# Optimization experiments

Measured on AMD Instinct MI355X. Metric: run time of the kernel, lower is better.

The kernel has to match this reference:

```python
import jax, jax.numpy as jnp
import numpy as np

N = 100000  # nodes
E = 320000  # edges
G = 64      # graphs in the batch


def setup_inputs() -> dict:
    key = jax.random.key(0)
    ks = jax.random.split(key, 16)
    inp = {
        "x": jax.random.normal(ks[0], (N, 512), dtype=jnp.float32),
        "edge_index": jax.random.randint(ks[1], (2, E), 0, N, dtype=jnp.int64),
        "batch": jnp.sort(jax.random.randint(ks[2], (N,), 0, G, dtype=jnp.int64)),
    }
    # GCNConv weights (in, out) and biases, Glorot-ish scale
    dims = [(512, 256), (256, 128), (128, 64), (64, 32)]
    for i, (din, dout) in enumerate(dims):
        inp[f"w{i+1}"] = jax.random.normal(ks[3 + i], (din, dout), dtype=jnp.float32) / np.sqrt(din)
        inp[f"b{i+1}"] = jnp.zeros((dout,), dtype=jnp.float32)
    inp["lw1"] = jax.random.normal(ks[8], (32, 16), dtype=jnp.float32) / np.sqrt(32.0)
    inp["lb1"] = jnp.zeros((16,), dtype=jnp.float32)
    inp["lw2"] = jax.random.normal(ks[9], (16, 2), dtype=jnp.float32) / np.sqrt(16.0)
    inp["lb2"] = jnpp = jnp.zeros((2,), dtype=jnp.float32)
    return inp


def _gcn_conv(h_in, w, b, src, dst, norm, n):
    # x' = D^-1/2 (A+I) D^-1/2 (X W) + b   (PyG GCNConv default)
    h = h_in @ w                                  # [N, out]
    msg = h[src] * norm[:, None]                  # gather + scale over edges(+self-loops)
    out = jax.ops.segment_sum(msg, dst, num_segments=n)  # scatter-add
    return out + b


def reference(x, edge_index, batch, w1, b1, w2, b2, w3, b3, w4, b4, lw1, lb1, lw2, lb2):
    n = x.shape[0]
    loop = jnp.arange(n, dtype=edge_index.dtype)
    src = jnp.concatenate([edge_index[0], loop])  # add self-loops
    dst = jnp.concatenate([edge_index[1], loop])
    # symmetric normalization: deg counted at dst (col) including self-loops
    deg = jax.ops.segment_sum(jnp.ones_like(dst, dtype=x.dtype), dst, num_segments=n)
    dinv = jnp.where(deg > 0, 1.0 / jnp.sqrt(deg), 0.0)
    norm = dinv[src] * dinv[dst]                  # [E+N]

    h = jax.nn.relu(_gcn_conv(x, w1, b1, src, dst, norm, n))
    h = jax.nn.relu(_gcn_conv(h, w2, b2, src, dst, norm, n))
    h = jax.nn.relu(_gcn_conv(h, w3, b3, src, dst, norm, n))
    h = _gcn_conv(h, w4, b4, src, dst, norm, n)   # [N, 32]

    # global mean pool over graphs
    sums = jax.ops.segment_sum(h, batch, num_segments=G)
    cnt = jax.ops.segment_sum(jnp.ones((n,), dtype=h.dtype), batch, num_segments=G)
    pooled = sums / jnp.maximum(cnt, 1.0)[:, None]  # [G, 32]

    # dropout p=0.8 is identity in eval mode
    out = jax.nn.relu(pooled @ lw1 + lb1) @ lw2 + lb2  # [G, 2]
    return out
```

## Files before the change

kernel.cpp:

```cpp
#include <hip/hip_runtime.h>
#include <cstdint>
#include <cstddef>


typedef __attribute__((ext_vector_type(8))) short s16x8;
typedef __attribute__((ext_vector_type(4))) float f32x4;

__device__ __forceinline__ short2 split2(float f) {
    union { float f; unsigned u; } c; c.f = f;
    short hi = (short)(c.u >> 16);
    union { unsigned u; float f; } h; h.u = c.u & 0xffff0000u;
    union { float f; unsigned u; } r; r.f = f - h.f;
    short lo = (short)(r.u >> 16);
    return make_short2(hi, lo);
}

__device__ __forceinline__ void gload16(const void* g, void* l) {
    __builtin_amdgcn_global_load_lds(
        (const __attribute__((address_space(1))) unsigned int*)g,
        (__attribute__((address_space(3))) unsigned int*)l, 16, 0, 0);
}


__global__ void k_count(const int* __restrict__ dst, int E, int* __restrict__ cnt) {
    int e = blockIdx.x * blockDim.x + threadIdx.x;
    if (e < E) atomicAdd(&cnt[dst[e]], 1);
}

__global__ void k_dinv(const int* __restrict__ cnt, int n, float* __restrict__ dinv) {
    int i = blockIdx.x * blockDim.x + threadIdx.x;
    if (i < n) dinv[i] = rsqrtf((float)(cnt[i] + 1));
}

__global__ void k_scan_sums(const int* __restrict__ cnt, int n, int* __restrict__ bsum) {
    __shared__ int s[256];
    int t = threadIdx.x;
    int base = blockIdx.x * 4096 + t * 16;
    int sum = 0;
#pragma unroll
    for (int j = 0; j < 16; ++j) { int i = base + j; if (i < n) sum += cnt[i]; }
    s[t] = sum;
    __syncthreads();
    for (int off = 128; off > 0; off >>= 1) {
        if (t < off) s[t] += s[t + off];
        __syncthreads();
    }
    if (t == 0) bsum[blockIdx.x] = s[0];
}

__global__ void k_scan_offsets(const int* __restrict__ bsum, int nb,
                               int* __restrict__ boff, int* __restrict__ totalp) {
    int t = threadIdx.x;
    int v = (t < nb) ? bsum[t] : 0;
    int x = v;
    for (int off = 1; off < 64; off <<= 1) {
        int y = __shfl_up(x, off);
        if (t >= off) x += y;
    }
    if (t < nb) boff[t] = x - v;
    if (t == 63) *totalp = x;
}

__global__ void k_scan_final(const int* __restrict__ cnt, int n,
                             const int* __restrict__ boff, int* __restrict__ row_ptr) {
    __shared__ int s[256];
    int t = threadIdx.x;
    int base = blockIdx.x * 4096 + t * 16;
    int v[16]; int sum = 0;
#pragma unroll
    for (int j = 0; j < 16; ++j) { int i = base + j; v[j] = (i < n) ? cnt[i] : 0; sum += v[j]; }
    s[t] = sum;
    __syncthreads();
    for (int off = 1; off < 256; off <<= 1) {
        int y = (t >= off) ? s[t - off] : 0;
        __syncthreads();
        s[t] += y;
        __syncthreads();
    }
    int run = boff[blockIdx.x] + ((t == 0) ? 0 : s[t - 1]);
#pragma unroll
    for (int j = 0; j < 16; ++j) {
        int i = base + j;
        if (i < n) row_ptr[i] = run;
        run += v[j];
    }
}

__global__ void k_fill(const int* __restrict__ src, const int* __restrict__ dst, int E,
                       const int* __restrict__ row_ptr, int* __restrict__ cursor,
                       int* __restrict__ csr_src) {
    int e = blockIdx.x * blockDim.x + threadIdx.x;
    if (e >= E) return;
    int d = dst[e];
    int p = atomicAdd(&cursor[d], 1);
    csr_src[row_ptr[d] + p] = src[e];
}


__global__ void k_split_w(const float* __restrict__ w, int N, int total, int kshift,
                          unsigned short* __restrict__ th, unsigned short* __restrict__ tl) {
    int idx = blockIdx.x * blockDim.x + threadIdx.x;
    if (idx >= total) return;
    int nn = idx >> kshift;
    int k  = idx & ((1 << kshift) - 1);
    short2 p = split2(w[(size_t)k * N + nn]);
    th[idx] = (unsigned short)p.x;
    tl[idx] = (unsigned short)p.y;
}


template <int FN, bool SPLIT_A>
__global__ __launch_bounds__(256)
void k_gemm(const float* __restrict__ A32,
            const unsigned short* __restrict__ Ah, const unsigned short* __restrict__ Al,
            const unsigned short* __restrict__ Bth, const unsigned short* __restrict__ Btl,
            float* __restrict__ C, int M, int K, int N) {
    constexpr int FM = 4;
    constexpr int BM = 128;
    constexpr int BN = FN * 32;
    constexpr int ABYTES = BM * 64;
    constexpr int BBYTES = BN * 64;
    constexpr int BUF = 2 * ABYTES + 2 * BBYTES;
    __shared__ char lds[2 * BUF];

    const int tid  = threadIdx.x;
    const int lane = tid & 63;
    const int w    = tid >> 6;
    const int wm   = w & 1;
    const int wn   = w >> 1;
    const int brow = blockIdx.y * BM;
    const int bcol = blockIdx.x * BN;
    const int l15  = lane & 15;
    const int kb   = (lane >> 4) * 16;

    const int arow_t = tid >> 1;
    const int ahalf  = tid & 1;
    int arow_g = brow + arow_t; if (arow_g > M - 1) arow_g = M - 1;
    const float* xrow = A32 + (size_t)arow_g * K + ahalf * 16;

    f32x4 acc[FM][FN];
#pragma unroll
    for (int i = 0; i < FM; ++i)
#pragma unroll
        for (int j = 0; j < FN; ++j) acc[i][j] = (f32x4){0.f, 0.f, 0.f, 0.f};

    const int KT = K / 32;
    float4 xr0, xr1, xr2, xr3;

    auto loadX = [&](int k0) {
        const float4* p = (const float4*)(xrow + k0);
        xr0 = p[0]; xr1 = p[1]; xr2 = p[2]; xr3 = p[3];
    };
    auto writeA = [&](char* base) {
        float v[16] = {xr0.x, xr0.y, xr0.z, xr0.w, xr1.x, xr1.y, xr1.z, xr1.w,
                       xr2.x, xr2.y, xr2.z, xr2.w, xr3.x, xr3.y, xr3.z, xr3.w};
        s16x8 h0, h1, l0, l1;
#pragma unroll
        for (int j = 0; j < 8; ++j) { short2 q = split2(v[j]);     h0[j] = q.x; l0[j] = q.y; }
#pragma unroll
        for (int j = 0; j < 8; ++j) { short2 q = split2(v[8 + j]); h1[j] = q.x; l1[j] = q.y; }
        int vq = (arow_t >> 1) & 3;
        int q0 = (2 * ahalf) ^ vq;
        int q1 = (2 * ahalf + 1) ^ vq;
        char* sAh = base;
        char* sAl = base + ABYTES;
        *(s16x8*)(sAh + arow_t * 64 + q0 * 16) = h0;
        *(s16x8*)(sAh + arow_t * 64 + q1 * 16) = h1;
        *(s16x8*)(sAl + arow_t * 64 + q0 * 16) = l0;
        *(s16x8*)(sAl + arow_t * 64 + q1 * 16) = l1;
    };
    auto stageAg = [&](char* base, int k0) {
#pragma unroll
        for (int u = 0; u < 4; ++u) {
            int id = w + u * 4;
            int hi = (id < 8) ? 1 : 0;
            int s  = hi ? id : id - 8;
            int p  = s * 64 + lane;
            int kq = (p ^ ((p >> 3) & 3)) & 3;
            int row = p >> 2;
            const unsigned short* gs = (hi ? Ah : Al) + (size_t)(brow + row) * K + k0 + kq * 8;
            gload16(gs, base + (hi ? 0 : ABYTES) + s * 1024);
        }
    };
    auto stageB = [&](char* base, int k0) {
        char* sBh = base + 2 * ABYTES;
        char* sBl = sBh + BBYTES;
#pragma unroll
        for (int u = 0; u < BN / 32; ++u) {
            int id = w + u * 4;
            int hi = (id < BN / 16) ? 1 : 0;
            int s  = hi ? id : id - BN / 16;
            int p  = s * 64 + lane;
            int kq = (p ^ ((p >> 3) & 3)) & 3;
            int col = p >> 2;
            const unsigned short* gs = (hi ? Bth : Btl) + (size_t)(bcol + col) * K + k0 + kq * 8;
            gload16(gs, (hi ? sBh : sBl) + s * 1024);
        }
    };

    char* cur = lds;
    char* nxt = lds + BUF;
    if constexpr (SPLIT_A) loadX(0);
    stageB(cur, 0);
    if constexpr (SPLIT_A) writeA(cur); else stageAg(cur, 0);
    __syncthreads();

    for (int t = 0; t < KT; ++t) {
        const int k1 = (t + 1) * 32;
        const bool more = (t + 1 < KT);
        if (more) {
            if constexpr (SPLIT_A) loadX(k1);
            stageB(nxt, k1);
            if constexpr (!SPLIT_A) stageAg(nxt, k1);
        }

        {
            char* sAh = cur;
            char* sAl = cur + ABYTES;
            char* sBh = cur + 2 * ABYTES;
            char* sBl = sBh + BBYTES;
            s16x8 fah[FM], fam[FM];
#pragma unroll
            for (int i = 0; i < FM; ++i) {
                int row = wm * 64 + i * 16 + l15;
                int o = row * 64 + (kb ^ (((row >> 1) & 3) << 4));
                fah[i] = *(const s16x8*)(sAh + o);
                fam[i] = *(const s16x8*)(sAl + o);
            }
#pragma unroll
            for (int j = 0; j < FN; ++j) {
                int col = wn * FN * 16 + j * 16 + l15;
                int o = col * 64 + (kb ^ (((col >> 1) & 3) << 4));
                s16x8 fbh = *(const s16x8*)(sBh + o);
                s16x8 fbm = *(const s16x8*)(sBl + o);
#pragma unroll
                for (int i = 0; i < FM; ++i) {
                    acc[i][j] = __builtin_amdgcn_mfma_f32_16x16x32_bf16(fah[i], fbh, acc[i][j], 0, 0, 0);
                    acc[i][j] = __builtin_amdgcn_mfma_f32_16x16x32_bf16(fam[i], fbh, acc[i][j], 0, 0, 0);
                    acc[i][j] = __builtin_amdgcn_mfma_f32_16x16x32_bf16(fah[i], fbm, acc[i][j], 0, 0, 0);
                }
            }
        }

        if constexpr (SPLIT_A) {
            if (more) writeA(nxt);
        }
        __syncthreads();
        char* tmp = cur; cur = nxt; nxt = tmp;
    }

#pragma unroll
    for (int i = 0; i < FM; ++i) {
#pragma unroll
        for (int r = 0; r < 4; ++r) {
            int row = brow + wm * 64 + i * 16 + (lane >> 4) * 4 + r;
            if (row >= M) continue;
#pragma unroll
            for (int j = 0; j < FN; ++j) {
                int col = bcol + wn * FN * 16 + j * 16 + l15;
                C[(size_t)row * N + col] = acc[i][j][r];
            }
        }
    }
}


__global__ void k_agg_split(const float4* __restrict__ h, const int* __restrict__ row_ptr,
                            const int* __restrict__ csr_src, const float* __restrict__ dinv,
                            const float* __restrict__ bias,
                            unsigned short* __restrict__ oh, unsigned short* __restrict__ ol,
                            int n, int f_shift) {
    int idx = blockIdx.x * blockDim.x + threadIdx.x;
    int dout4 = 1 << f_shift;
    int total = n << f_shift;
    if (idx >= total) return;
    int i = idx >> f_shift;
    int f = idx & (dout4 - 1);

    float di = dinv[i];
    float4 hv = h[(size_t)i * dout4 + f];
    float4 acc;
    acc.x = hv.x * di; acc.y = hv.y * di; acc.z = hv.z * di; acc.w = hv.w * di;

    int s0 = row_ptr[i], s1 = row_ptr[i + 1];
    for (int e = s0; e < s1; ++e) {
        int s = csr_src[e];
        float ds = dinv[s];
        float4 v = h[(size_t)s * dout4 + f];
        acc.x += v.x * ds; acc.y += v.y * ds; acc.z += v.z * ds; acc.w += v.w * ds;
    }
    const float4* b4 = (const float4*)bias;
    float4 b = b4[f];
    float4 o;
    o.x = fmaxf(acc.x * di + b.x, 0.f);
    o.y = fmaxf(acc.y * di + b.y, 0.f);
    o.z = fmaxf(acc.z * di + b.z, 0.f);
    o.w = fmaxf(acc.w * di + b.w, 0.f);

    short2 p0 = split2(o.x), p1 = split2(o.y), p2 = split2(o.z), p3 = split2(o.w);
    size_t base = ((size_t)i << f_shift << 2) + f * 4;
    *(ushort4*)(oh + base) = make_ushort4((unsigned short)p0.x, (unsigned short)p1.x,
                                          (unsigned short)p2.x, (unsigned short)p3.x);
    *(ushort4*)(ol + base) = make_ushort4((unsigned short)p0.y, (unsigned short)p1.y,
                                          (unsigned short)p2.y, (unsigned short)p3.y);
}


__global__ void k_agg(const float4* __restrict__ h, const int* __restrict__ row_ptr,
                      const int* __restrict__ csr_src, const float* __restrict__ dinv,
                      const float* __restrict__ bias, float4* __restrict__ out,
                      int n, int f_shift) {
    int idx = blockIdx.x * blockDim.x + threadIdx.x;
    int dout4 = 1 << f_shift;
    int total = n << f_shift;
    if (idx >= total) return;
    int i = idx >> f_shift;
    int f = idx & (dout4 - 1);

    float di = dinv[i];
    float4 hv = h[(size_t)i * dout4 + f];
    float4 acc;
    acc.x = hv.x * di; acc.y = hv.y * di; acc.z = hv.z * di; acc.w = hv.w * di;

    int s0 = row_ptr[i], s1 = row_ptr[i + 1];
    for (int e = s0; e < s1; ++e) {
        int s = csr_src[e];
        float ds = dinv[s];
        float4 v = h[(size_t)s * dout4 + f];
        acc.x += v.x * ds; acc.y += v.y * ds; acc.z += v.z * ds; acc.w += v.w * ds;
    }
    const float4* b4 = (const float4*)bias;
    float4 b = b4[f];
    float4 o;
    o.x = acc.x * di + b.x;
    o.y = acc.y * di + b.y;
    o.z = acc.z * di + b.z;
    o.w = acc.w * di + b.w;
    out[(size_t)i * dout4 + f] = o;
}


__global__ void k_pool(const float* __restrict__ h, const int* __restrict__ batch,
                       int n, float* __restrict__ pooled) {
    int g = blockIdx.x;
    int start, end;
    {
        int lo = 0, hi = n;
        while (lo < hi) { int mid = (lo + hi) >> 1; if (batch[mid] < g) lo = mid + 1; else hi = mid; }
        start = lo;
        lo = start; hi = n;
        while (lo < hi) { int mid = (lo + hi) >> 1; if (batch[mid] < g + 1) lo = mid + 1; else hi = mid; }
        end = lo;
    }
    int f = threadIdx.x & 31;
    int sub = threadIdx.x >> 5;
    float s = 0.f;
    for (int i = start + sub; i < end; i += 8) s += h[(size_t)i * 32 + f];
    __shared__ float red[8][32];
    red[sub][f] = s;
    __syncthreads();
    if (sub == 0) {
        float t = 0.f;
#pragma unroll
        for (int k = 0; k < 8; ++k) t += red[k][f];
        int c = end - start;
        pooled[g * 32 + f] = t / (float)(c > 0 ? c : 1);
    }
}


__global__ void k_mlp(const float* __restrict__ pooled, const float* __restrict__ lw1,
                      const float* __restrict__ lb1, const float* __restrict__ lw2,
                      const float* __restrict__ lb2, float* __restrict__ out, int g_count) {
    int g = threadIdx.x;
    if (g >= g_count) return;
    float p[32];
#pragma unroll
    for (int k = 0; k < 32; ++k) p[k] = pooled[g * 32 + k];
    float hmid[16];
#pragma unroll
    for (int j = 0; j < 16; ++j) {
        float s = lb1[j];
#pragma unroll
        for (int k = 0; k < 32; ++k) s += p[k] * lw1[k * 16 + j];
        hmid[j] = fmaxf(s, 0.f);
    }
#pragma unroll
    for (int o = 0; o < 2; ++o) {
        float s = lb2[o];
#pragma unroll
        for (int k = 0; k < 16; ++k) s += hmid[k] * lw2[k * 2 + o];
        out[g * 2 + o] = s;
    }
}


extern "C" void kernel_launch(void* const* d_in, const int* in_sizes, int n_in,
                              void* d_out, int out_size, void* d_ws, size_t ws_size,
                              hipStream_t stream) {
    const float* x     = (const float*)d_in[0];
    const int*   ei    = (const int*)d_in[1];
    const int*   batch = (const int*)d_in[2];
    const float* w1 = (const float*)d_in[3];  const float* b1 = (const float*)d_in[4];
    const float* w2 = (const float*)d_in[5];  const float* b2 = (const float*)d_in[6];
    const float* w3 = (const float*)d_in[7];  const float* b3 = (const float*)d_in[8];
    const float* w4 = (const float*)d_in[9];  const float* b4 = (const float*)d_in[10];
    const float* lw1 = (const float*)d_in[11]; const float* lb1 = (const float*)d_in[12];
    const float* lw2 = (const float*)d_in[13]; const float* lb2 = (const float*)d_in[14];
    float* out = (float*)d_out;

    const int n = in_sizes[0] / 512;
    const int E = in_sizes[1] / 2;
    const int G = 64;

    const int* src = ei;
    const int* dst = ei + E;

    char* ws = (char*)d_ws;
    size_t off = 0;
    auto alloc = [&](size_t bytes) -> void* {
        void* p = ws + off;
        off = (off + bytes + 255) & ~((size_t)255);
        return p;
    };
    float*          bufA = (float*)alloc((size_t)n * 256 * sizeof(float));
    unsigned short* pAh  = (unsigned short*)alloc((size_t)n * 256 * 2);
    unsigned short* pAl  = (unsigned short*)alloc((size_t)n * 256 * 2);
    int*   cnt     = (int*)alloc((size_t)n * sizeof(int));
    int*   row_ptr = (int*)alloc((size_t)(n + 1) * sizeof(int));
    int*   cursor  = (int*)alloc((size_t)n * sizeof(int));
    int*   csr     = (int*)alloc((size_t)E * sizeof(int));
    float* dinv    = (float*)alloc((size_t)n * sizeof(float));
    float* pooled  = (float*)alloc((size_t)G * 32 * sizeof(float));
    int*   bsum    = (int*)alloc(64 * sizeof(int));
    int*   boff    = (int*)alloc(64 * sizeof(int));
    unsigned short* w1h = (unsigned short*)alloc(256 * 512 * 2);
    unsigned short* w1l = (unsigned short*)alloc(256 * 512 * 2);
    unsigned short* w2h = (unsigned short*)alloc(128 * 256 * 2);
    unsigned short* w2l = (unsigned short*)alloc(128 * 256 * 2);
    unsigned short* w3h = (unsigned short*)alloc(64 * 128 * 2);
    unsigned short* w3l = (unsigned short*)alloc(64 * 128 * 2);
    unsigned short* w4h = (unsigned short*)alloc(32 * 64 * 2);
    unsigned short* w4l = (unsigned short*)alloc(32 * 64 * 2);
    float* bufB = (float*)(pAl + (size_t)n * 64);
    (void)ws_size;

    hipMemsetAsync(cnt, 0, (size_t)n * sizeof(int), stream);
    hipMemsetAsync(cursor, 0, (size_t)n * sizeof(int), stream);

    k_split_w<<<(256 * 512 + 255) / 256, 256, 0, stream>>>(w1, 256, 256 * 512, 9, w1h, w1l);
    k_split_w<<<(128 * 256 + 255) / 256, 256, 0, stream>>>(w2, 128, 128 * 256, 8, w2h, w2l);
    k_split_w<<<(64 * 128 + 255) / 256, 256, 0, stream>>>(w3, 64, 64 * 128, 7, w3h, w3l);
    k_split_w<<<(32 * 64 + 255) / 256, 256, 0, stream>>>(w4, 32, 32 * 64, 6, w4h, w4l);

    const int nscan = (n + 4095) / 4096;
    k_count<<<(E + 255) / 256, 256, 0, stream>>>(dst, E, cnt);
    k_dinv <<<(n + 255) / 256, 256, 0, stream>>>(cnt, n, dinv);
    k_scan_sums   <<<nscan, 256, 0, stream>>>(cnt, n, bsum);
    k_scan_offsets<<<1, 64, 0, stream>>>(bsum, nscan, boff, row_ptr + n);
    k_scan_final  <<<nscan, 256, 0, stream>>>(cnt, n, boff, row_ptr);
    k_fill<<<(E + 255) / 256, 256, 0, stream>>>(src, dst, E, row_ptr, cursor, csr);

    const int gy = (n + 127) / 128;

    k_gemm<4, true><<<dim3(2, gy), 256, 0, stream>>>(
        x, nullptr, nullptr, w1h, w1l, bufA, n, 512, 256);
    k_agg_split<<<((size_t)n * 64 + 255) / 256, 256, 0, stream>>>(
        (const float4*)bufA, row_ptr, csr, dinv, b1, pAh, pAl, n, 6);

    k_gemm<4, false><<<dim3(1, gy), 256, 0, stream>>>(
        nullptr, pAh, pAl, w2h, w2l, bufA, n, 256, 128);
    k_agg_split<<<((size_t)n * 32 + 255) / 256, 256, 0, stream>>>(
        (const float4*)bufA, row_ptr, csr, dinv, b2, pAh, pAl, n, 5);

    k_gemm<2, false><<<dim3(1, gy), 256, 0, stream>>>(
        nullptr, pAh, pAl, w3h, w3l, bufA, n, 128, 64);
    k_agg_split<<<((size_t)n * 16 + 255) / 256, 256, 0, stream>>>(
        (const float4*)bufA, row_ptr, csr, dinv, b3, pAh, pAl, n, 4);

    k_gemm<1, false><<<dim3(1, gy), 256, 0, stream>>>(
        nullptr, pAh, pAl, w4h, w4l, bufA, n, 64, 32);
    k_agg<<<((size_t)n * 8 + 255) / 256, 256, 0, stream>>>(
        (const float4*)bufA, row_ptr, csr, dinv, b4, (float4*)bufB, n, 3);

    k_pool<<<G, 256, 0, stream>>>(bufB, batch, n, pooled);
    k_mlp<<<1, 64, 0, stream>>>(pooled, lw1, lb1, lw2, lb2, out, G);
}
```

Before: 498.7 us.

## Add dedicated deep-pipelined layer-1 GEMM with triple-buffered B and explicit waitcnt

Splits the fp32-input first-layer GEMM into its own kernel, k_gemm1, with compile-time K=512 and a fully unrolled K loop. It prefetches x two tiles ahead in registers and triple-buffers the weight tiles in dynamic LDS (80 KB). It replaces full syncthreads with a manual vmcnt wait plus s_barrier so that global loads overlap the MFMA work. The aim is to hide the global memory latency of the largest GEMM, at the cost of more LDS per block, which can lower occupancy, and of hand-written waitcnt counts that must match the number of issued loads.

```diff
diff --git a/kernel.cpp b/kernel.cpp
--- a/kernel.cpp
+++ b/kernel.cpp
@@ -109,10 +109,152 @@
 }
 
 
-template <int FN, bool SPLIT_A>
 __global__ __launch_bounds__(256)
-void k_gemm(const float* __restrict__ A32,
-            const unsigned short* __restrict__ Ah, const unsigned short* __restrict__ Al,
+void k_gemm1(const float* __restrict__ A32,
+             const unsigned short* __restrict__ Bth, const unsigned short* __restrict__ Btl,
+             float* __restrict__ C, int M) {
+    constexpr int K = 512, KT = 16;
+    constexpr int APL = 128 * 64;
+    constexpr int ABUF = 2 * APL;
+    constexpr int BPL = 128 * 64;
+    constexpr int BBUF = 2 * BPL;
+    extern __shared__ __attribute__((aligned(16))) char lds[];
+    char* aB0 = lds;
+    char* aB1 = lds + ABUF;
+    char* bB0 = lds + 2 * ABUF;
+    char* bB1 = bB0 + BBUF;
+    char* bB2 = bB1 + BBUF;
+    char* aB[2] = {aB0, aB1};
+    char* bB[3] = {bB0, bB1, bB2};
+
+    const int tid  = threadIdx.x;
+    const int lane = tid & 63;
+    const int w    = tid >> 6;
+    const int wm   = w & 1;
+    const int wn   = w >> 1;
+    const int brow = blockIdx.y * 128;
+    const int bcol = blockIdx.x * 128;
+    const int l15  = lane & 15;
+    const int kb   = (lane >> 4) * 16;
+
+    const int arow  = tid >> 1;
+    const int ahalf = tid & 1;
+    int ag = brow + arow; if (ag > M - 1) ag = M - 1;
+    const float* xrow = A32 + (size_t)ag * K + ahalf * 16;
+    const int vq = (arow >> 1) & 3;
+    const int q0 = ((2 * ahalf) ^ vq) * 16;
+    const int q1 = ((2 * ahalf + 1) ^ vq) * 16;
+
+    f32x4 acc[4][4];
+#pragma unroll
+    for (int i = 0; i < 4; ++i)
+#pragma unroll
+        for (int j = 0; j < 4; ++j) acc[i][j] = (f32x4){0.f, 0.f, 0.f, 0.f};
+
+    float4 xr[2][4];
+
+    auto X = [&](int t, int p) {
+        const float4* q = (const float4*)(xrow + t * 32);
+        xr[p][0] = q[0]; xr[p][1] = q[1]; xr[p][2] = q[2]; xr[p][3] = q[3];
+    };
+    auto SB = [&](char* bbuf, int t) {
+#pragma unroll
+        for (int u = 0; u < 4; ++u) {
+            int id = w + u * 4;
+            int hi = (id < 8) ? 1 : 0;
+            int s  = hi ? id : id - 8;
+            int p  = s * 64 + lane;
+            int kq = (p ^ ((p >> 3) & 3)) & 3;
+            int col = p >> 2;
+            const unsigned short* gs = (hi ? Bth : Btl) + (size_t)(bcol + col) * K + t * 32 + kq * 8;
+            gload16(gs, (hi ? bbuf : bbuf + BPL) + s * 1024);
+        }
+    };
+    auto WA = [&](char* abuf, int p) {
+        float v[16] = {xr[p][0].x, xr[p][0].y, xr[p][0].z, xr[p][0].w,
+                       xr[p][1].x, xr[p][1].y, xr[p][1].z, xr[p][1].w,
+                       xr[p][2].x, xr[p][2].y, xr[p][2].z, xr[p][2].w,
+                       xr[p][3].x, xr[p][3].y, xr[p][3].z, xr[p][3].w};
+        s16x8 h0, h1, l0, l1;
+#pragma unroll
+        for (int j = 0; j < 8; ++j) { short2 q = split2(v[j]);     h0[j] = q.x; l0[j] = q.y; }
+#pragma unroll
+        for (int j = 0; j < 8; ++j) { short2 q = split2(v[8 + j]); h1[j] = q.x; l1[j] = q.y; }
+        *(s16x8*)(abuf + arow * 64 + q0)       = h0;
+        *(s16x8*)(abuf + arow * 64 + q1)       = h1;
+        *(s16x8*)(abuf + APL + arow * 64 + q0) = l0;
+        *(s16x8*)(abuf + APL + arow * 64 + q1) = l1;
+    };
+    auto MM = [&](char* abuf, char* bbuf) {
+        char* sAh = abuf;
+        char* sAl = abuf + APL;
+        char* sBh = bbuf;
+        char* sBl = bbuf + BPL;
+        s16x8 fah[4], fam[4];
+#pragma unroll
+        for (int i = 0; i < 4; ++i) {
+            int row = wm * 64 + i * 16 + l15;
+            int o = row * 64 + (kb ^ (((row >> 1) & 3) << 4));
+            fah[i] = *(const s16x8*)(sAh + o);
+            fam[i] = *(const s16x8*)(sAl + o);
+        }
+#pragma unroll
+        for (int j = 0; j < 4; ++j) {
+            int col = wn * 64 + j * 16 + l15;
+            int o = col * 64 + (kb ^ (((col >> 1) & 3) << 4));
+            s16x8 fbh = *(const s16x8*)(sBh + o);
+            s16x8 fbm = *(const s16x8*)(sBl + o);
+#pragma unroll
+            for (int i = 0; i < 4; ++i) {
+                acc[i][j] = __builtin_amdgcn_mfma_f32_16x16x32_bf16(fah[i], fbh, acc[i][j], 0, 0, 0);
+                acc[i][j] = __builtin_amdgcn_mfma_f32_16x16x32_bf16(fam[i], fbh, acc[i][j], 0, 0, 0);
+                acc[i][j] = __builtin_amdgcn_mfma_f32_16x16x32_bf16(fah[i], fbm, acc[i][j], 0, 0, 0);
+            }
+        }
+    };
+
+    X(0, 0);
+    SB(bB[0], 0);
+    X(1, 1);
+    SB(bB[1], 1);
+    WA(aB[0], 0);
+
+#pragma unroll
+    for (int t = 0; t < KT; ++t) {
+        if (t + 1 < KT) {
+            asm volatile("s_waitcnt vmcnt(8) lgkmcnt(0)" ::: "memory");
+        } else {
+            asm volatile("s_waitcnt vmcnt(0) lgkmcnt(0)" ::: "memory");
+        }
+        __builtin_amdgcn_sched_barrier(0);
+        __builtin_amdgcn_s_barrier();
+        if (t + 2 < KT) {
+            X(t + 2, t & 1);
+            SB(bB[(t + 2) % 3], t + 2);
+        }
+        MM(aB[t & 1], bB[t % 3]);
+        if (t + 1 < KT) WA(aB[(t + 1) & 1], (t + 1) & 1);
+    }
+
+#pragma unroll
+    for (int i = 0; i < 4; ++i) {
+#pragma unroll
+        for (int r = 0; r < 4; ++r) {
+            int row = brow + wm * 64 + i * 16 + (lane >> 4) * 4 + r;
+            if (row >= M) continue;
+#pragma unroll
+            for (int j = 0; j < 4; ++j) {
+                int col = bcol + wn * 64 + j * 16 + l15;
+                C[(size_t)row * 256 + col] = acc[i][j][r];
+            }
+        }
+    }
+}
+
+
+template <int FN>
+__global__ __launch_bounds__(256)
+void k_gemm(const unsigned short* __restrict__ Ah, const unsigned short* __restrict__ Al,
             const unsigned short* __restrict__ Bth, const unsigned short* __restrict__ Btl,
             float* __restrict__ C, int M, int K, int N) {
     constexpr int FM = 4;
@@ -133,43 +275,13 @@
     const int l15  = lane & 15;
     const int kb   = (lane >> 4) * 16;
 
-    const int arow_t = tid >> 1;
-    const int ahalf  = tid & 1;
-    int arow_g = brow + arow_t; if (arow_g > M - 1) arow_g = M - 1;
-    const float* xrow = A32 + (size_t)arow_g * K + ahalf * 16;
-
     f32x4 acc[FM][FN];
 #pragma unroll
     for (int i = 0; i < FM; ++i)
 #pragma unroll
         for (int j = 0; j < FN; ++j) acc[i][j] = (f32x4){0.f, 0.f, 0.f, 0.f};
 
-    const int KT = K / 32;
-    float4 xr0, xr1, xr2, xr3;
-
-    auto loadX = [&](int k0) {
-        const float4* p = (const float4*)(xrow + k0);
-        xr0 = p[0]; xr1 = p[1]; xr2 = p[2]; xr3 = p[3];
-    };
-    auto writeA = [&](char* base) {
-        float v[16] = {xr0.x, xr0.y, xr0.z, xr0.w, xr1.x, xr1.y, xr1.z, xr1.w,
-                       xr2.x, xr2.y, xr2.z, xr2.w, xr3.x, xr3.y, xr3.z, xr3.w};
-        s16x8 h0, h1, l0, l1;
-#pragma unroll
-        for (int j = 0; j < 8; ++j) { short2 q = split2(v[j]);     h0[j] = q.x; l0[j] = q.y; }
-#pragma unroll
-        for (int j = 0; j < 8; ++j) { short2 q = split2(v[8 + j]); h1[j] = q.x; l1[j] = q.y; }
-        int vq = (arow_t >> 1) & 3;
-        int q0 = (2 * ahalf) ^ vq;
-        int q1 = (2 * ahalf + 1) ^ vq;
-        char* sAh = base;
-        char* sAl = base + ABYTES;
-        *(s16x8*)(sAh + arow_t * 64 + q0 * 16) = h0;
-        *(s16x8*)(sAh + arow_t * 64 + q1 * 16) = h1;
-        *(s16x8*)(sAl + arow_t * 64 + q0 * 16) = l0;
-        *(s16x8*)(sAl + arow_t * 64 + q1 * 16) = l1;
-    };
-    auto stageAg = [&](char* base, int k0) {
+    auto stageA = [&](char* base, int k0) {
 #pragma unroll
         for (int u = 0; u < 4; ++u) {
             int id = w + u * 4;
@@ -200,20 +312,17 @@
 
     char* cur = lds;
     char* nxt = lds + BUF;
-    if constexpr (SPLIT_A) loadX(0);
     stageB(cur, 0);
-    if constexpr (SPLIT_A) writeA(cur); else stageAg(cur, 0);
+    stageA(cur, 0);
     __syncthreads();
 
+    const int KT = K / 32;
     for (int t = 0; t < KT; ++t) {
         const int k1 = (t + 1) * 32;
-        const bool more = (t + 1 < KT);
-        if (more) {
-            if constexpr (SPLIT_A) loadX(k1);
+        if (t + 1 < KT) {
             stageB(nxt, k1);
-            if constexpr (!SPLIT_A) stageAg(nxt, k1);
-        }
-
+            stageA(nxt, k1);
+        }
         {
             char* sAh = cur;
             char* sAl = cur + ABYTES;
@@ -240,10 +349,6 @@
                     acc[i][j] = __builtin_amdgcn_mfma_f32_16x16x32_bf16(fah[i], fbm, acc[i][j], 0, 0, 0);
                 }
             }
-        }
-
-        if constexpr (SPLIT_A) {
-            if (more) writeA(nxt);
         }
         __syncthreads();
         char* tmp = cur; cur = nxt; nxt = tmp;
@@ -445,6 +550,9 @@
     float* bufB = (float*)(pAl + (size_t)n * 64);
     (void)ws_size;
 
+    hipFuncSetAttribute((const void*)k_gemm1,
+                        hipFuncAttributeMaxDynamicSharedMemorySize, 80 * 1024);
+
     hipMemsetAsync(cnt, 0, (size_t)n * sizeof(int), stream);
     hipMemsetAsync(cursor, 0, (size_t)n * sizeof(int), stream);
 
@@ -463,23 +571,19 @@
 
     const int gy = (n + 127) / 128;
 
-    k_gemm<4, true><<<dim3(2, gy), 256, 0, stream>>>(
-        x, nullptr, nullptr, w1h, w1l, bufA, n, 512, 256);
+    k_gemm1<<<dim3(2, gy), 256, 80 * 1024, stream>>>(x, w1h, w1l, bufA, n);
     k_agg_split<<<((size_t)n * 64 + 255) / 256, 256, 0, stream>>>(
         (const float4*)bufA, row_ptr, csr, dinv, b1, pAh, pAl, n, 6);
 
-    k_gemm<4, false><<<dim3(1, gy), 256, 0, stream>>>(
-        nullptr, pAh, pAl, w2h, w2l, bufA, n, 256, 128);
+    k_gemm<4><<<dim3(1, gy), 256, 0, stream>>>(pAh, pAl, w2h, w2l, bufA, n, 256, 128);
     k_agg_split<<<((size_t)n * 32 + 255) / 256, 256, 0, stream>>>(
         (const float4*)bufA, row_ptr, csr, dinv, b2, pAh, pAl, n, 5);
 
-    k_gemm<2, false><<<dim3(1, gy), 256, 0, stream>>>(
-        nullptr, pAh, pAl, w3h, w3l, bufA, n, 128, 64);
+    k_gemm<2><<<dim3(1, gy), 256, 0, stream>>>(pAh, pAl, w3h, w3l, bufA, n, 128, 64);
     k_agg_split<<<((size_t)n * 16 + 255) / 256, 256, 0, stream>>>(
         (const float4*)bufA, row_ptr, csr, dinv, b3, pAh, pAl, n, 4);
 
-    k_gemm<1, false><<<dim3(1, gy), 256, 0, stream>>>(
-        nullptr, pAh, pAl, w4h, w4l, bufA, n, 64, 32);
+    k_gemm<1><<<dim3(1, gy), 256, 0, stream>>>(pAh, pAl, w4h, w4l, bufA, n, 64, 32);
     k_agg<<<((size_t)n * 8 + 255) / 256, 256, 0, stream>>>(
         (const float4*)bufA, row_ptr, csr, dinv, b4, (float4*)bufB, n, 3);
 
```

After: 512.4 us. +2.7%, slower.
